# Kernel optimization log

Measured on AMD Instinct MI355X. Metric: run time of the kernel, lower is better.

The kernel has to match this reference:

```python
import jax, jax.numpy as jnp
import numpy as np
import math

D_MODEL = 2048
N_HEADS = 16
BATCH = 2
SEQ = 2048
ALIBI_BIAS_MAX = 8


def alibi_bias(n_heads, seq_len, alibi_bias_max=8):
    # matches torch alibi_bias(full=False): shape [1, n_heads, 1, seq_len]
    dist = jnp.arange(1 - seq_len, 1, dtype=jnp.float32).reshape(1, 1, 1, seq_len)
    m = jnp.arange(1, n_heads + 1, dtype=jnp.float32) * (alibi_bias_max / n_heads)
    slopes = 1.0 / (2.0 ** m).reshape(1, n_heads, 1, 1)
    return dist * slopes


def setup_inputs() -> dict:
    key = jax.random.key(0)
    ks = jax.random.split(key, 5)
    d = D_MODEL
    scale = 1.0 / math.sqrt(d)
    x = jax.random.normal(ks[0], (BATCH, SEQ, d), dtype=jnp.float32)
    w_qkv = jax.random.normal(ks[1], (3 * d, d), dtype=jnp.float32) * scale
    b_qkv = jnp.zeros((3 * d,), dtype=jnp.float32)
    w_out = jax.random.normal(ks[2], (d, d), dtype=jnp.float32) * scale
    b_out = jnp.zeros((d,), dtype=jnp.float32)
    attn_mask = alibi_bias(N_HEADS, SEQ, ALIBI_BIAS_MAX)
    return {"x": x, "attn_mask": attn_mask, "w_qkv": w_qkv, "b_qkv": b_qkv,
            "w_out": w_out, "b_out": b_out}


def reference(x, attn_mask, w_qkv, b_qkv, w_out, b_out):
    B, S, D = x.shape
    H = N_HEADS
    hd = D // H
    # packed QKV projection
    qkv = x @ w_qkv.T + b_qkv                      # [B,S,3D]
    qkv = qkv.reshape(B, S, 3, H, hd)
    q, k, v = qkv[:, :, 0], qkv[:, :, 1], qkv[:, :, 2]  # [B,S,H,hd]
    scores = jnp.einsum('bqhd,bkhd->bhqk', q, k) * (1.0 / math.sqrt(hd))
    scores = scores + attn_mask                    # ALiBi additive bias [1,H,1,S]
    causal = jnp.tril(jnp.ones((S, S), dtype=bool))
    scores = jnp.where(causal, scores, -jnp.inf)
    probs = jax.nn.softmax(scores, axis=-1)        # [B,H,S,S]
    ctx = jnp.einsum('bhqk,bkhd->bqhd', probs, v).reshape(B, S, D)
    return ctx @ w_out.T + b_out
```

## Files before the change

### kernel.cpp

```cpp
#include <hip/hip_runtime.h>
#include <math.h>

typedef unsigned short u16;
typedef __attribute__((ext_vector_type(8))) short short8;
typedef __attribute__((ext_vector_type(4))) float f32x4;

#define MFMA16x16x32(a, b, c) __builtin_amdgcn_mfma_f32_16x16x32_bf16((a), (b), (c), 0, 0, 0)
#define GLL16(g, s)                                                        \
  __builtin_amdgcn_global_load_lds(                                        \
      (const __attribute__((address_space(1))) void*)(g),                  \
      (__attribute__((address_space(3))) void*)(s), 16, 0, 0)

__device__ __forceinline__ u16 f32_to_bf16(float x) {
  union { float f; unsigned u; } v; v.f = x;
  unsigned r = v.u + 0x7FFFu + ((v.u >> 16) & 1u);
  return (u16)(r >> 16);
}

__global__ void cvt_f32_bf16(const float* __restrict__ in, u16* __restrict__ out, int n4) {
  int i = blockIdx.x * blockDim.x + threadIdx.x;
  int stride = gridDim.x * blockDim.x;
  for (; i < n4; i += stride) {
    float4 v = ((const float4*)in)[i];
    ushort4 o;
    o.x = f32_to_bf16(v.x);
    o.y = f32_to_bf16(v.y);
    o.z = f32_to_bf16(v.z);
    o.w = f32_to_bf16(v.w);
    ((ushort4*)out)[i] = o;
  }
}

template <int OUT_BF16>
__global__ __launch_bounds__(512, 2) void gemm_nt_8p(
    const u16* __restrict__ A,
    const u16* __restrict__ B,
    const float* __restrict__ bias,
    void* __restrict__ C,
    int M, int N, int K)
{
  __shared__ u16 As[2][8192];
  __shared__ u16 Bs[2][16384];

  const int tid = threadIdx.x;
  const int w = tid >> 6, l = tid & 63;
  const int l15 = l & 15, l4 = l >> 4;
  const int wm = w >> 2, wn = w & 3;
  const long bm = (long)blockIdx.y * 128, bn = (long)blockIdx.x * 256;
  const int NT = K >> 6;

  const u16 *aSrc0, *aSrc1, *bSrc0, *bSrc1;
  {
    int q = w * 2048 + l * 16;
    int r = q >> 7, cb = (q & 127) ^ ((r & 7) << 4);
    aSrc0 = A + (bm + r) * (long)K + (cb >> 1);
    bSrc0 = B + (bn + r) * (long)K + (cb >> 1);
    q += 1024;
    r = q >> 7; cb = (q & 127) ^ ((r & 7) << 4);
    aSrc1 = A + (bm + r) * (long)K + (cb >> 1);
    bSrc1 = B + (bn + r) * (long)K + (cb >> 1);
  }
  const long bHS = 128 * (long)K;
  const int ldsA = w * 1024;

  const f32x4 z4 = {0.f, 0.f, 0.f, 0.f};
  f32x4 acc[4][4];
  #pragma unroll
  for (int m = 0; m < 4; ++m)
    #pragma unroll
    for (int n = 0; n < 4; ++n) acc[m][n] = z4;

  const int xo0 = (l4 * 16) ^ ((l15 & 7) << 4);
  const int xo1 = (64 + l4 * 16) ^ ((l15 & 7) << 4);
  const char* aRd = (const char*)&As[0][0] + (wm * 64 + l15) * 128;
  const char* bRd = (const char*)&Bs[0][0] + (wn * 32 + l15) * 128;

  GLL16(aSrc0, &As[0][ldsA]);
  GLL16(aSrc1, &As[0][ldsA + 512]);
  GLL16(bSrc0, &Bs[0][ldsA]);
  GLL16(bSrc1, &Bs[0][ldsA + 512]);
  GLL16(bSrc0 + bHS, &Bs[0][8192 + ldsA]);
  GLL16(bSrc1 + bHS, &Bs[0][8192 + ldsA + 512]);

  short8 af[4][2], bf[4][2];

  for (int t = 0; t < NT; ++t) {
    const int nxt = t + 1;
    const int bufo = t & 1;

    if (nxt < NT) {
      const long ko = (long)nxt * 64;
      const int nb = nxt & 1;
      GLL16(aSrc0 + ko, &As[nb][ldsA]);
      GLL16(aSrc1 + ko, &As[nb][ldsA + 512]);
      GLL16(bSrc0 + ko, &Bs[nb][ldsA]);
      GLL16(bSrc1 + ko, &Bs[nb][ldsA + 512]);
      asm volatile("s_waitcnt vmcnt(6)\ns_barrier" ::: "memory");
    } else {
      asm volatile("s_waitcnt vmcnt(2)\ns_barrier" ::: "memory");
    }
    const char* ab = aRd + bufo * 16384;
    const char* bb = bRd + bufo * 32768;
    #pragma unroll
    for (int m = 0; m < 4; ++m) {
      af[m][0] = *(const short8*)(ab + m * 2048 + xo0);
      af[m][1] = *(const short8*)(ab + m * 2048 + xo1);
    }
    #pragma unroll
    for (int n = 0; n < 2; ++n) {
      bf[n][0] = *(const short8*)(bb + n * 2048 + xo0);
      bf[n][1] = *(const short8*)(bb + n * 2048 + xo1);
    }
    __builtin_amdgcn_s_setprio(1);
    #pragma unroll
    for (int m = 0; m < 4; ++m)
      #pragma unroll
      for (int n = 0; n < 2; ++n) {
        acc[m][n] = MFMA16x16x32(af[m][0], bf[n][0], acc[m][n]);
        acc[m][n] = MFMA16x16x32(af[m][1], bf[n][1], acc[m][n]);
      }
    __builtin_amdgcn_s_setprio(0);

    if (nxt < NT) {
      const long ko = (long)nxt * 64;
      const int nb = nxt & 1;
      GLL16(bSrc0 + bHS + ko, &Bs[nb][8192 + ldsA]);
      GLL16(bSrc1 + bHS + ko, &Bs[nb][8192 + ldsA + 512]);
      asm volatile("s_waitcnt vmcnt(6)\ns_barrier" ::: "memory");
    } else {
      asm volatile("s_waitcnt vmcnt(0)\ns_barrier" ::: "memory");
    }
    const char* bb1 = bb + 16384;
    #pragma unroll
    for (int n = 0; n < 2; ++n) {
      bf[2 + n][0] = *(const short8*)(bb1 + n * 2048 + xo0);
      bf[2 + n][1] = *(const short8*)(bb1 + n * 2048 + xo1);
    }
    __builtin_amdgcn_s_setprio(1);
    #pragma unroll
    for (int m = 0; m < 4; ++m)
      #pragma unroll
      for (int n = 2; n < 4; ++n) {
        acc[m][n] = MFMA16x16x32(af[m][0], bf[n][0], acc[m][n]);
        acc[m][n] = MFMA16x16x32(af[m][1], bf[n][1], acc[m][n]);
      }
    __builtin_amdgcn_s_setprio(0);
  }

  #pragma unroll
  for (int m = 0; m < 4; ++m) {
    const long row0 = bm + wm * 64 + m * 16 + l4 * 4;
    #pragma unroll
    for (int n = 0; n < 4; ++n) {
      const long col = bn + wn * 32 + (n & 1) * 16 + (n >> 1) * 128 + l15;
      const float bv = bias[col];
      #pragma unroll
      for (int r = 0; r < 4; ++r) {
        const float v = acc[m][n][r] + bv;
        if (OUT_BF16)
          ((u16*)C)[(row0 + r) * (long)N + col] = f32_to_bf16(v);
        else
          ((float*)C)[(row0 + r) * (long)N + col] = v;
      }
    }
  }
}

__global__ __launch_bounds__(256) void repack_kv(
    const u16* __restrict__ qkv, u16* __restrict__ kimg, u16* __restrict__ vimg)
{
  const int t = blockIdx.x;
  const int h = blockIdx.y, b = blockIdx.z;
  const int tid = threadIdx.x;
  __shared__ u16 Vl[64][136];

  const long qbase = ((long)(b * 2048 + t * 64)) * 6144 + h * 128;
  u16* kout = kimg + (((long)(b * 16 + h) * 32 + t) * 8192);
  u16* vout = vimg + (((long)(b * 16 + h) * 32 + t) * 8192);

  #pragma unroll
  for (int i = 0; i < 4; ++i) {
    const int j = tid + i * 256;
    {
      const int r = j >> 4, c8 = (j & 15) * 8;
      uint4 v = *(const uint4*)(qkv + qbase + (long)r * 6144 + 4096 + c8);
      *(uint4*)(&Vl[r][c8]) = v;
    }
    {
      const int byte = j * 16;
      const int r = byte >> 8;
      const int wv = (byte & 255) ^ ((r & 7) << 4);
      const int d0 = wv >> 1;
      uint4 v = *(const uint4*)(qkv + qbase + (long)r * 6144 + 2048 + d0);
      *(uint4*)(kout + j * 8) = v;
    }
  }
  __syncthreads();
  #pragma unroll
  for (int i = 0; i < 4; ++i) {
    const int j = tid + i * 256;
    const int byte = j * 16;
    const int d = byte >> 7;
    const int wv = (byte & 127) ^ ((d & 7) << 4);
    const int k0 = wv >> 1;
    u16 tmp[8];
    #pragma unroll
    for (int m = 0; m < 8; ++m) tmp[m] = Vl[k0 + m][d];
    *(uint4*)(vout + j * 8) = *(const uint4*)tmp;
  }
}

__global__ __launch_bounds__(256) void attn_kernel(
    const u16* __restrict__ qkv,
    const u16* __restrict__ kimg,
    const u16* __restrict__ vimg,
    u16* __restrict__ ctx)
{
  const int S = 2048, NHD = 6144, NT = 32;
  const int p = blockIdx.x, h = blockIdx.y, b = blockIdx.z;
  const int tid = threadIdx.x;
  const int w = tid >> 6, l = tid & 63;
  const int l15 = l & 15, l4 = l >> 4;

  __shared__ u16 Ks[64 * 128];
  __shared__ u16 Vt[128 * 64];
  __shared__ u16 Ps[4][16 * 64];

  const float LOG2E = 1.44269504088896f;
  const float c1 = 0.08838834764831845f * LOG2E;
  const float slope2 = exp2f(-0.5f * (float)(h + 1)) * LOG2E;

  const f32x4 z4 = {0.f, 0.f, 0.f, 0.f};

  for (int pass = 0; pass < 2; ++pass) {
    const int qblk = pass ? (NT - 1 - p) : p;
    const int qb0 = qblk * 64;

    short8 qf[4];
    {
      const int qrow = qb0 + w * 16 + l15;
      const u16* qp = qkv + (long)(b * S + qrow) * NHD + h * 128 + l4 * 8;
      #pragma unroll
      for (int kc = 0; kc < 4; ++kc) qf[kc] = *(const short8*)(qp + kc * 32);
    }

    f32x4 o[8];
    #pragma unroll
    for (int i = 0; i < 8; ++i) o[i] = z4;
    float m_r[4] = {-3.0e38f, -3.0e38f, -3.0e38f, -3.0e38f};
    float l_r[4] = {0.f, 0.f, 0.f, 0.f};

    for (int kt = 0; kt <= qblk; ++kt) {
      const u16* ksrc = kimg + (((long)(b * 16 + h) * NT + kt) * 8192);
      const u16* vsrc = vimg + (((long)(b * 16 + h) * NT + kt) * 8192);
      #pragma unroll
      for (int i = 0; i < 4; ++i) {
        const int chunk = w * 4 + i;
        __builtin_amdgcn_global_load_lds(
            (const __attribute__((address_space(1))) void*)(ksrc + chunk * 512 + l * 8),
            (__attribute__((address_space(3))) void*)(Ks + chunk * 512), 16, 0, 0);
        __builtin_amdgcn_global_load_lds(
            (const __attribute__((address_space(1))) void*)(vsrc + chunk * 512 + l * 8),
            (__attribute__((address_space(3))) void*)(Vt + chunk * 512), 16, 0, 0);
      }
      __syncthreads();

      f32x4 sf[4];
      #pragma unroll
      for (int nt = 0; nt < 4; ++nt) sf[nt] = z4;
      #pragma unroll
      for (int nt = 0; nt < 4; ++nt) {
        const int krow = nt * 16 + l15;
        #pragma unroll
        for (int kc = 0; kc < 4; ++kc) {
          int kbyte = (krow * 256 + kc * 64 + l4 * 16) ^ ((krow & 7) << 4);
          const short8 kf = *(const short8*)((const char*)Ks + kbyte);
          sf[nt] = MFMA16x16x32(qf[kc], kf, sf[nt]);
        }
      }

      float add_nt[4];
      int kg_nt[4];
      #pragma unroll
      for (int nt = 0; nt < 4; ++nt) {
        kg_nt[nt] = kt * 64 + nt * 16 + l15;
        add_nt[nt] = slope2 * (float)(kg_nt[nt] - (S - 1));
      }
      const bool diag = (kt == qblk);
      float alpha[4];
      #pragma unroll
      for (int r = 0; r < 4; ++r) {
        const int qrow_l = l4 * 4 + r;
        const int qg = qb0 + w * 16 + qrow_l;
        float sc[4];
        #pragma unroll
        for (int nt = 0; nt < 4; ++nt) sc[nt] = sf[nt][r] * c1 + add_nt[nt];
        if (diag) {
          #pragma unroll
          for (int nt = 0; nt < 4; ++nt)
            if (kg_nt[nt] > qg) sc[nt] = -3.0e38f;
        }
        float mx = fmaxf(fmaxf(sc[0], sc[1]), fmaxf(sc[2], sc[3]));
        #pragma unroll
        for (int d = 1; d < 16; d <<= 1) mx = fmaxf(mx, __shfl_xor(mx, d, 64));
        const float mnew = fmaxf(m_r[r], mx);
        float sum = 0.f;
        #pragma unroll
        for (int nt = 0; nt < 4; ++nt) {
          const float pv = exp2f(sc[nt] - mnew);
          sc[nt] = pv;
          sum += pv;
        }
        #pragma unroll
        for (int d = 1; d < 16; d <<= 1) sum += __shfl_xor(sum, d, 64);
        alpha[r] = exp2f(m_r[r] - mnew);
        l_r[r] = l_r[r] * alpha[r] + sum;
        m_r[r] = mnew;
        #pragma unroll
        for (int nt = 0; nt < 4; ++nt) {
          int pbyte = ((qrow_l * 64 + nt * 16 + l15) * 2) ^ ((qrow_l & 7) << 4);
          *(u16*)((char*)&Ps[w][0] + pbyte) = f32_to_bf16(sc[nt]);
        }
      }

      #pragma unroll
      for (int nt = 0; nt < 8; ++nt)
        #pragma unroll
        for (int r = 0; r < 4; ++r) o[nt][r] *= alpha[r];

      #pragma unroll
      for (int kc = 0; kc < 2; ++kc) {
        int pbyte = ((l15 * 64 + kc * 32 + l4 * 8) * 2) ^ ((l15 & 7) << 4);
        const short8 pf = *(const short8*)((const char*)&Ps[w][0] + pbyte);
        #pragma unroll
        for (int nt = 0; nt < 8; ++nt) {
          const int d = nt * 16 + l15;
          const int vbyte = ((d * 128 + kc * 64 + l4 * 16)) ^ ((d & 7) << 4);
          const short8 vf = *(const short8*)((const char*)Vt + vbyte);
          o[nt] = MFMA16x16x32(pf, vf, o[nt]);
        }
      }
      __syncthreads();
    }

    float rl[4];
    #pragma unroll
    for (int r = 0; r < 4; ++r) rl[r] = 1.0f / l_r[r];
    #pragma unroll
    for (int nt = 0; nt < 8; ++nt) {
      #pragma unroll
      for (int r = 0; r < 4; ++r) {
        const int qg = qb0 + w * 16 + l4 * 4 + r;
        ctx[(long)(b * S + qg) * 2048 + h * 128 + nt * 16 + l15] =
            f32_to_bf16(o[nt][r] * rl[r]);
      }
    }
  }
}

extern "C" void kernel_launch(void* const* d_in, const int* in_sizes, int n_in,
                              void* d_out, int out_size, void* d_ws, size_t ws_size,
                              hipStream_t stream) {
  const float* x     = (const float*)d_in[0];
  const float* w_qkv = (const float*)d_in[2];
  const float* b_qkv = (const float*)d_in[3];
  const float* w_out = (const float*)d_in[4];
  const float* b_out = (const float*)d_in[5];
  float* out = (float*)d_out;

  char* ws = (char*)d_ws;
  u16* xb    = (u16*)(ws);
  u16* wqkvb = (u16*)(ws + 16777216UL);
  u16* woutb = (u16*)(ws + 41943040UL);
  u16* qkvb  = (u16*)(ws + 50331648UL);
  u16* ctxb  = (u16*)(ws + 100663296UL);
  u16* kimg  = (u16*)(ws);
  u16* vimg  = (u16*)(ws + 16777216UL);

  cvt_f32_bf16<<<2048, 256, 0, stream>>>(x, xb, 8388608 / 4);
  cvt_f32_bf16<<<2048, 256, 0, stream>>>(w_qkv, wqkvb, 12582912 / 4);
  cvt_f32_bf16<<<2048, 256, 0, stream>>>(w_out, woutb, 4194304 / 4);

  gemm_nt_8p<1><<<dim3(24, 32), 512, 0, stream>>>(xb, wqkvb, b_qkv, (void*)qkvb, 4096, 6144, 2048);

  repack_kv<<<dim3(32, 16, 2), 256, 0, stream>>>(qkvb, kimg, vimg);

  attn_kernel<<<dim3(16, 16, 2), 256, 0, stream>>>(qkvb, kimg, vimg, ctxb);

  gemm_nt_8p<0><<<dim3(8, 32), 512, 0, stream>>>(ctxb, woutb, b_out, (void*)out, 4096, 2048, 2048);
}
```

Baseline: 309.9 us.

## Use 256x256 tiled GEMM with staged half-tile prefetch for QKV projection

Adds a new GEMM kernel that computes 256x256 output tiles per block instead of 128x256, and uses it for the QKV projection. Its loop is split into four phases, each loading A and B half-tiles through global_load_lds with interleaved barriers and MFMA priority raises, so loads overlap compute. The larger tile raises arithmetic intensity and cuts global traffic, but halves the grid to 384 blocks and increases LDS use, which may lower occupancy. The output projection still uses the old kernel.

```diff
diff --git a/kernel.cpp b/kernel.cpp
--- a/kernel.cpp
+++ b/kernel.cpp
@@ -32,16 +32,169 @@
 }
 
 template <int OUT_BF16>
-__global__ __launch_bounds__(512, 2) void gemm_nt_8p(
+__global__ __launch_bounds__(512, 2) void gemm_nt_256(
     const u16* __restrict__ A,
     const u16* __restrict__ B,
     const float* __restrict__ bias,
     void* __restrict__ C,
     int M, int N, int K)
 {
+  __shared__ u16 As[2][2][8192];
+  __shared__ u16 Bs[2][2][8192];
+
+  const int tid = threadIdx.x;
+  const int w = tid >> 6, l = tid & 63;
+  const int l15 = l & 15, l4 = l >> 4;
+  const int wm = w >> 2, wn = w & 3;
+  const long bm = (long)blockIdx.y * 256, bn = (long)blockIdx.x * 256;
+  const int NT = K >> 6;
+
+  const int r0 = tid >> 3;
+  const int cb0 = ((tid * 16) & 127) ^ ((r0 & 7) << 4);
+  const u16* aS = A + (bm + r0) * (long)K + (cb0 >> 1);
+  const u16* bS = B + (bn + r0) * (long)K + (cb0 >> 1);
+  const long rK64 = 64 * (long)K, rK128 = 128 * (long)K;
+  const int ldst = w * 512;
+
+#define STG_A(buf, half, tt)                                                   \
+  do {                                                                         \
+    GLL16(aS + (half) * rK128 + (long)(tt) * 64, &As[buf][half][ldst]);        \
+    GLL16(aS + (half) * rK128 + rK64 + (long)(tt) * 64,                        \
+          &As[buf][half][ldst + 4096]);                                        \
+  } while (0)
+#define STG_B(buf, half, tt)                                                   \
+  do {                                                                         \
+    GLL16(bS + (half) * rK128 + (long)(tt) * 64, &Bs[buf][half][ldst]);        \
+    GLL16(bS + (half) * rK128 + rK64 + (long)(tt) * 64,                        \
+          &Bs[buf][half][ldst + 4096]);                                        \
+  } while (0)
+
+  const f32x4 z4 = {0.f, 0.f, 0.f, 0.f};
+  f32x4 acc[8][4];
+  #pragma unroll
+  for (int m = 0; m < 8; ++m)
+    #pragma unroll
+    for (int n = 0; n < 4; ++n) acc[m][n] = z4;
+
+  const int swz = (l15 & 7) << 4;
+  const int xo0 = (l4 * 16) ^ swz;
+  const int xo1 = (64 + l4 * 16) ^ swz;
+
+  short8 af[4][2], bf[4][2];
+
+  STG_A(0, 0, 0); STG_A(0, 1, 0);
+  STG_B(0, 0, 0); STG_B(0, 1, 0);
+  STG_B(1, 0, 1); STG_B(1, 1, 1);
+
+  for (int t = 0; t < NT; ++t) {
+    const int bufo = t & 1, nb = bufo ^ 1;
+    const char* aH = (const char*)&As[bufo][wm][0] + l15 * 128;
+    const char* bH = (const char*)&Bs[bufo][wn >> 1][0] + ((wn & 1) * 64 + l15) * 128;
+
+    if (t + 1 < NT) STG_A(nb, 0, t + 1);
+    if (t == NT - 1) asm volatile("s_waitcnt vmcnt(0)" ::: "memory");
+    else             asm volatile("s_waitcnt vmcnt(6)" ::: "memory");
+    __builtin_amdgcn_s_barrier();
+    #pragma unroll
+    for (int m = 0; m < 4; ++m) {
+      af[m][0] = *(const short8*)(aH + m * 2048 + xo0);
+      af[m][1] = *(const short8*)(aH + m * 2048 + xo1);
+    }
+    #pragma unroll
+    for (int n = 0; n < 2; ++n) {
+      bf[n][0] = *(const short8*)(bH + n * 2048 + xo0);
+      bf[n][1] = *(const short8*)(bH + n * 2048 + xo1);
+    }
+    __builtin_amdgcn_s_setprio(1);
+    #pragma unroll
+    for (int m = 0; m < 4; ++m)
+      #pragma unroll
+      for (int n = 0; n < 2; ++n) {
+        acc[m][n] = MFMA16x16x32(af[m][0], bf[n][0], acc[m][n]);
+        acc[m][n] = MFMA16x16x32(af[m][1], bf[n][1], acc[m][n]);
+      }
+    __builtin_amdgcn_s_setprio(0);
+    __builtin_amdgcn_s_barrier();
+
+    if (t + 1 < NT) STG_A(nb, 1, t + 1);
+    __builtin_amdgcn_s_barrier();
+    #pragma unroll
+    for (int n = 0; n < 2; ++n) {
+      bf[2 + n][0] = *(const short8*)(bH + (2 + n) * 2048 + xo0);
+      bf[2 + n][1] = *(const short8*)(bH + (2 + n) * 2048 + xo1);
+    }
+    __builtin_amdgcn_s_setprio(1);
+    #pragma unroll
+    for (int m = 0; m < 4; ++m)
+      #pragma unroll
+      for (int n = 2; n < 4; ++n) {
+        acc[m][n] = MFMA16x16x32(af[m][0], bf[n][0], acc[m][n]);
+        acc[m][n] = MFMA16x16x32(af[m][1], bf[n][1], acc[m][n]);
+      }
+    __builtin_amdgcn_s_setprio(0);
+    __builtin_amdgcn_s_barrier();
+
+    if (t + 2 < NT) STG_B(bufo, 0, t + 2);
+    __builtin_amdgcn_s_barrier();
+    #pragma unroll
+    for (int m = 0; m < 4; ++m) {
+      af[m][0] = *(const short8*)(aH + (4 + m) * 2048 + xo0);
+      af[m][1] = *(const short8*)(aH + (4 + m) * 2048 + xo1);
+    }
+    __builtin_amdgcn_s_setprio(1);
+    #pragma unroll
+    for (int m = 0; m < 4; ++m)
+      #pragma unroll
+      for (int n = 0; n < 2; ++n) {
+        acc[4 + m][n] = MFMA16x16x32(af[m][0], bf[n][0], acc[4 + m][n]);
+        acc[4 + m][n] = MFMA16x16x32(af[m][1], bf[n][1], acc[4 + m][n]);
+      }
+    __builtin_amdgcn_s_setprio(0);
+    __builtin_amdgcn_s_barrier();
+
+    if (t + 2 < NT) STG_B(bufo, 1, t + 2);
+    __builtin_amdgcn_s_barrier();
+    __builtin_amdgcn_s_setprio(1);
+    #pragma unroll
+    for (int m = 0; m < 4; ++m)
+      #pragma unroll
+      for (int n = 2; n < 4; ++n) {
+        acc[4 + m][n] = MFMA16x16x32(af[m][0], bf[n][0], acc[4 + m][n]);
+        acc[4 + m][n] = MFMA16x16x32(af[m][1], bf[n][1], acc[4 + m][n]);
+      }
+    __builtin_amdgcn_s_setprio(0);
+    __builtin_amdgcn_s_barrier();
+  }
+#undef STG_A
+#undef STG_B
+
+  #pragma unroll
+  for (int m = 0; m < 8; ++m) {
+    const long row0 = bm + wm * 128 + m * 16 + l4 * 4;
+    #pragma unroll
+    for (int n = 0; n < 4; ++n) {
+      const long col = bn + wn * 64 + n * 16 + l15;
+      const float bv = bias[col];
+      #pragma unroll
+      for (int r = 0; r < 4; ++r) {
+        const float v = acc[m][n][r] + bv;
+        if (OUT_BF16)
+          ((u16*)C)[(row0 + r) * (long)N + col] = f32_to_bf16(v);
+        else
+          ((float*)C)[(row0 + r) * (long)N + col] = v;
+      }
+    }
+  }
+}
+
+template <int OUT_BF16>
+__global__ __launch_bounds__(512, 2) void gemm_nt_8p(
+    const u16* __restrict__ A, const u16* __restrict__ B,
+    const float* __restrict__ bias, void* __restrict__ C,
+    int M, int N, int K)
+{
   __shared__ u16 As[2][8192];
   __shared__ u16 Bs[2][16384];
-
   const int tid = threadIdx.x;
   const int w = tid >> 6, l = tid & 63;
   const int l15 = l & 15, l4 = l >> 4;
@@ -381,7 +534,7 @@
   cvt_f32_bf16<<<2048, 256, 0, stream>>>(w_qkv, wqkvb, 12582912 / 4);
   cvt_f32_bf16<<<2048, 256, 0, stream>>>(w_out, woutb, 4194304 / 4);
 
-  gemm_nt_8p<1><<<dim3(24, 32), 512, 0, stream>>>(xb, wqkvb, b_qkv, (void*)qkvb, 4096, 6144, 2048);
+  gemm_nt_256<1><<<dim3(24, 16), 512, 0, stream>>>(xb, wqkvb, b_qkv, (void*)qkvb, 4096, 6144, 2048);
 
   repack_kv<<<dim3(32, 16, 2), 256, 0, stream>>>(qkvb, kimg, vimg);
 
```

After: 335.0 us. 8.1% more time.

## Deepen GEMM prefetch to two stages with a triple-buffered B tile

Applied to the files above, without the earlier changes.

Restructures the bf16 GEMM main loop so global-to-LDS loads are issued two k-tiles ahead. B gets a third LDS buffer and A stays double-buffered. All six loads for a tile are issued in one batch after the mid-iteration barrier, once the A fragments have been pulled into registers. The aim is to hide global load latency better and drop the split per-half waits of the previous schedule. The cost is more LDS per block (B buffers grow from 64KB to 96KB) and a new barrier/waitcnt ordering that must keep in-flight buffers from being overwritten.

```diff
diff --git a/kernel.cpp b/kernel.cpp
--- a/kernel.cpp
+++ b/kernel.cpp
@@ -32,7 +32,7 @@
 }
 
 template <int OUT_BF16>
-__global__ __launch_bounds__(512, 2) void gemm_nt_8p(
+__global__ __launch_bounds__(512, 2) void gemm_nt_p2(
     const u16* __restrict__ A,
     const u16* __restrict__ B,
     const float* __restrict__ bias,
@@ -40,7 +40,7 @@
     int M, int N, int K)
 {
   __shared__ u16 As[2][8192];
-  __shared__ u16 Bs[2][16384];
+  __shared__ u16 Bs[3][16384];
 
   const int tid = threadIdx.x;
   const int w = tid >> 6, l = tid & 63;
@@ -61,7 +61,19 @@
     bSrc1 = B + (bn + r) * (long)K + (cb >> 1);
   }
   const long bHS = 128 * (long)K;
-  const int ldsA = w * 1024;
+  const int ldst = w * 1024;
+
+#define STAGE6(tt)                                                            \
+  do {                                                                        \
+    const long ko = (long)(tt) * 64;                                          \
+    const int vb = (tt) % 3, ab = (tt) & 1;                                   \
+    GLL16(aSrc0 + ko, &As[ab][ldst]);                                         \
+    GLL16(aSrc1 + ko, &As[ab][ldst + 512]);                                   \
+    GLL16(bSrc0 + ko, &Bs[vb][ldst]);                                         \
+    GLL16(bSrc1 + ko, &Bs[vb][ldst + 512]);                                   \
+    GLL16(bSrc0 + bHS + ko, &Bs[vb][8192 + ldst]);                            \
+    GLL16(bSrc1 + bHS + ko, &Bs[vb][8192 + ldst + 512]);                      \
+  } while (0)
 
   const f32x4 z4 = {0.f, 0.f, 0.f, 0.f};
   f32x4 acc[4][4];
@@ -72,35 +84,17 @@
 
   const int xo0 = (l4 * 16) ^ ((l15 & 7) << 4);
   const int xo1 = (64 + l4 * 16) ^ ((l15 & 7) << 4);
-  const char* aRd = (const char*)&As[0][0] + (wm * 64 + l15) * 128;
-  const char* bRd = (const char*)&Bs[0][0] + (wn * 32 + l15) * 128;
-
-  GLL16(aSrc0, &As[0][ldsA]);
-  GLL16(aSrc1, &As[0][ldsA + 512]);
-  GLL16(bSrc0, &Bs[0][ldsA]);
-  GLL16(bSrc1, &Bs[0][ldsA + 512]);
-  GLL16(bSrc0 + bHS, &Bs[0][8192 + ldsA]);
-  GLL16(bSrc1 + bHS, &Bs[0][8192 + ldsA + 512]);
 
   short8 af[4][2], bf[4][2];
 
+  STAGE6(0);
+  STAGE6(1);
+  asm volatile("s_waitcnt vmcnt(6)\ns_barrier" ::: "memory");
+
   for (int t = 0; t < NT; ++t) {
-    const int nxt = t + 1;
-    const int bufo = t & 1;
-
-    if (nxt < NT) {
-      const long ko = (long)nxt * 64;
-      const int nb = nxt & 1;
-      GLL16(aSrc0 + ko, &As[nb][ldsA]);
-      GLL16(aSrc1 + ko, &As[nb][ldsA + 512]);
-      GLL16(bSrc0 + ko, &Bs[nb][ldsA]);
-      GLL16(bSrc1 + ko, &Bs[nb][ldsA + 512]);
-      asm volatile("s_waitcnt vmcnt(6)\ns_barrier" ::: "memory");
-    } else {
-      asm volatile("s_waitcnt vmcnt(2)\ns_barrier" ::: "memory");
-    }
-    const char* ab = aRd + bufo * 16384;
-    const char* bb = bRd + bufo * 32768;
+    const char* ab = (const char*)&As[t & 1][0] + (wm * 64 + l15) * 128;
+    const char* bb = (const char*)&Bs[t % 3][0] + (wn * 32 + l15) * 128;
+
     #pragma unroll
     for (int m = 0; m < 4; ++m) {
       af[m][0] = *(const short8*)(ab + m * 2048 + xo0);
@@ -111,6 +105,7 @@
       bf[n][0] = *(const short8*)(bb + n * 2048 + xo0);
       bf[n][1] = *(const short8*)(bb + n * 2048 + xo1);
     }
+    asm volatile("s_waitcnt lgkmcnt(0)" ::: "memory");
     __builtin_amdgcn_s_setprio(1);
     #pragma unroll
     for (int m = 0; m < 4; ++m)
@@ -120,22 +115,18 @@
         acc[m][n] = MFMA16x16x32(af[m][1], bf[n][1], acc[m][n]);
       }
     __builtin_amdgcn_s_setprio(0);
-
-    if (nxt < NT) {
-      const long ko = (long)nxt * 64;
-      const int nb = nxt & 1;
-      GLL16(bSrc0 + bHS + ko, &Bs[nb][8192 + ldsA]);
-      GLL16(bSrc1 + bHS + ko, &Bs[nb][8192 + ldsA + 512]);
-      asm volatile("s_waitcnt vmcnt(6)\ns_barrier" ::: "memory");
-    } else {
-      asm volatile("s_waitcnt vmcnt(0)\ns_barrier" ::: "memory");
-    }
-    const char* bb1 = bb + 16384;
+    asm volatile("s_barrier" ::: "memory");
+
     #pragma unroll
     for (int n = 0; n < 2; ++n) {
-      bf[2 + n][0] = *(const short8*)(bb1 + n * 2048 + xo0);
-      bf[2 + n][1] = *(const short8*)(bb1 + n * 2048 + xo1);
-    }
+      bf[2 + n][0] = *(const short8*)(bb + 16384 + n * 2048 + xo0);
+      bf[2 + n][1] = *(const short8*)(bb + 16384 + n * 2048 + xo1);
+    }
+    if (t + 2 < NT) STAGE6(t + 2);
+    if (t >= NT - 2)
+      asm volatile("s_waitcnt vmcnt(0) lgkmcnt(0)" ::: "memory");
+    else
+      asm volatile("s_waitcnt vmcnt(6) lgkmcnt(0)" ::: "memory");
     __builtin_amdgcn_s_setprio(1);
     #pragma unroll
     for (int m = 0; m < 4; ++m)
@@ -145,7 +136,9 @@
         acc[m][n] = MFMA16x16x32(af[m][1], bf[n][1], acc[m][n]);
       }
     __builtin_amdgcn_s_setprio(0);
-  }
+    asm volatile("s_barrier" ::: "memory");
+  }
+#undef STAGE6
 
   #pragma unroll
   for (int m = 0; m < 4; ++m) {
@@ -381,11 +374,11 @@
   cvt_f32_bf16<<<2048, 256, 0, stream>>>(w_qkv, wqkvb, 12582912 / 4);
   cvt_f32_bf16<<<2048, 256, 0, stream>>>(w_out, woutb, 4194304 / 4);
 
-  gemm_nt_8p<1><<<dim3(24, 32), 512, 0, stream>>>(xb, wqkvb, b_qkv, (void*)qkvb, 4096, 6144, 2048);
+  gemm_nt_p2<1><<<dim3(24, 32), 512, 0, stream>>>(xb, wqkvb, b_qkv, (void*)qkvb, 4096, 6144, 2048);
 
   repack_kv<<<dim3(32, 16, 2), 256, 0, stream>>>(qkvb, kimg, vimg);
 
   attn_kernel<<<dim3(16, 16, 2), 256, 0, stream>>>(qkvb, kimg, vimg, ctxb);
 
-  gemm_nt_8p<0><<<dim3(8, 32), 512, 0, stream>>>(ctxb, woutb, b_out, (void*)out, 4096, 2048, 2048);
-}
+  gemm_nt_p2<0><<<dim3(8, 32), 512, 0, stream>>>(ctxb, woutb, b_out, (void*)out, 4096, 2048, 2048);
+}
```

Result: no change. 307.3 us (-0.8%).
